# Performance work log

Hardware: AMD Instinct MI355X
Metric: run time of the kernel (lower is better)

## Reference

```python
import jax, jax.numpy as jnp
import numpy as np

D_MODEL = 1024
N_HEADS = 16
HEAD_DIM = D_MODEL // N_HEADS


def setup_inputs() -> dict:
    key = jax.random.key(0)
    ks = jax.random.split(key, 5)
    B, S = 2, 2048
    x = jax.random.normal(ks[0], (B, S, D_MODEL), dtype=jnp.float32)
    # nn.Linear weights: [out_features, in_features]
    s_in = 1.0 / np.sqrt(D_MODEL)
    qkv_w = jax.random.uniform(ks[1], (3 * D_MODEL, D_MODEL), jnp.float32, -s_in, s_in)
    qkv_b = jax.random.uniform(ks[2], (3 * D_MODEL,), jnp.float32, -s_in, s_in)
    out_w = jax.random.uniform(ks[3], (D_MODEL, D_MODEL), jnp.float32, -s_in, s_in)
    out_b = jax.random.uniform(ks[4], (D_MODEL,), jnp.float32, -s_in, s_in)
    return {"x": x, "qkv_w": qkv_w, "qkv_b": qkv_b, "out_w": out_w, "out_b": out_b}


def reference(x, qkv_w, qkv_b, out_w, out_b):
    B, S, D = x.shape
    H, Hd = N_HEADS, HEAD_DIM
    scale = 1.0 / np.sqrt(Hd)
    qkv = jnp.einsum('bsd,ed->bse', x, qkv_w) + qkv_b  # [B,S,3D]
    qkv = qkv.reshape(B, S, 3, H, Hd)
    q = qkv[:, :, 0].transpose(0, 2, 1, 3)  # [B,H,S,Hd]
    k = qkv[:, :, 1].transpose(0, 2, 1, 3)
    v = qkv[:, :, 2].transpose(0, 2, 1, 3)
    scores = jnp.einsum('bhqd,bhkd->bhqk', q, k) * scale  # [B,H,S,S]
    causal = jnp.triu(jnp.ones((S, S), dtype=bool), k=1)
    scores = jnp.where(causal[None, None], -jnp.inf, scores)
    probs = jax.nn.softmax(scores, axis=-1)
    out = jnp.einsum('bhqk,bhkd->bhqd', probs, v)  # [B,H,S,Hd]
    out = out.transpose(0, 2, 1, 3).reshape(B, S, D)
    out = jnp.einsum('bsd,ed->bse', out, out_w) + out_b
    return out
```

## Files before the change

kernel.cpp:

```cpp
#include <hip/hip_runtime.h>
#include <hip/hip_bf16.h>

#define SEQ    2048
#define DMODEL 1024
#define NHEAD  16
#define HDIM   64
#define BATCH  2
#define NTOK   (BATCH * SEQ)

#define N_X   (NTOK * DMODEL)
#define N_WQ  (3 * DMODEL * DMODEL)
#define N_BQ  (3 * DMODEL)
#define N_WO  (DMODEL * DMODEL)
#define N_BO  (DMODEL)
#define N_CANON (N_X + N_WQ + N_BQ + N_WO + N_BO)

#define NEG_SENT (-1.0e30f)
#define QSCALE 0.1803368801111f

typedef __attribute__((ext_vector_type(8))) short short8;
typedef __attribute__((ext_vector_type(4))) short short4v;
typedef __attribute__((ext_vector_type(4))) float f32x4;

#define MFMA_BF16(A, B, C) __builtin_amdgcn_mfma_f32_16x16x32_bf16((A), (B), (C), 0, 0, 0)

static __device__ __forceinline__ short8 load8(const __hip_bfloat16* p) {
    return *(const short8*)p;
}

static __device__ __forceinline__ void async16(const void* g, void* l) {
    __builtin_amdgcn_global_load_lds(
        (const __attribute__((address_space(1))) unsigned int*)g,
        (__attribute__((address_space(3))) unsigned int*)l,
        16, 0, 0);
}

__global__ void detect_kernel(const unsigned short* __restrict__ w, int* flag) {
    int cnt = 0;
    for (int i = threadIdx.x; i < 512; i += 64) {
        const unsigned e = (w[i] >> 7) & 0xFF;
        if (e >= 125) cnt++;
    }
#pragma unroll
    for (int o = 32; o; o >>= 1) cnt += __shfl_down(cnt, o);
    if (threadIdx.x == 0) *flag = (cnt > 8) ? 1 : 0;
}

__global__ __launch_bounds__(256) void canon_kernel(
    const void* __restrict__ s0, const void* __restrict__ s1,
    const void* __restrict__ s2, const void* __restrict__ s3,
    const void* __restrict__ s4,
    __hip_bfloat16* __restrict__ dst, const int* __restrict__ flag)
{
    const int idx = blockIdx.x * 256 + threadIdx.x;
    if (idx >= N_CANON) return;
    const void* src;
    int off;
    if (idx < N_X)                         { src = s0; off = idx; }
    else if (idx < N_X + N_WQ)             { src = s1; off = idx - N_X; }
    else if (idx < N_X + N_WQ + N_BQ)      { src = s2; off = idx - (N_X + N_WQ); }
    else if (idx < N_X + N_WQ + N_BQ + N_WO){ src = s3; off = idx - (N_X + N_WQ + N_BQ); }
    else                                   { src = s4; off = idx - (N_X + N_WQ + N_BQ + N_WO); }
    const bool isf32 = (*flag != 0);
    const float v = isf32 ? ((const float*)src)[off]
                          : __bfloat162float(((const __hip_bfloat16*)src)[off]);
    dst[idx] = __float2bfloat16(v);
}

__global__ __launch_bounds__(256) void qkv_gemm_kernel(
    const __hip_bfloat16* __restrict__ X,
    const __hip_bfloat16* __restrict__ W,
    const __hip_bfloat16* __restrict__ bias,
    __hip_bfloat16* __restrict__ Qs,
    __hip_bfloat16* __restrict__ Kb,
    __hip_bfloat16* __restrict__ Vt)
{
    constexpr int Kd = DMODEL;
    __shared__ __align__(16) __hip_bfloat16 As[2][128 * 32];
    __shared__ __align__(16) __hip_bfloat16 Bs[2][128 * 32];

    const int tid   = threadIdx.x;
    const int lane  = tid & 63;
    const int w     = tid >> 6;
    const int mTile = blockIdx.y * 128;
    const int nTile = blockIdx.x * 128;
    const int wm    = (w >> 1) * 64;
    const int wn    = (w & 1) * 64;
    const int lm    = lane & 15;
    const int lk    = (lane >> 4) * 8;

    f32x4 acc[4][4];
#pragma unroll
    for (int i = 0; i < 4; ++i)
#pragma unroll
        for (int j = 0; j < 4; ++j)
            acc[i][j] = (f32x4){0.f, 0.f, 0.f, 0.f};

    const int r0c = tid >> 2, p0c = tid & 3;
    const int r1c = (tid + 256) >> 2;

    const __hip_bfloat16* gA0 = &X[(size_t)(mTile + r0c) * Kd + p0c * 8];
    const __hip_bfloat16* gA1 = &X[(size_t)(mTile + r1c) * Kd + p0c * 8];
    const __hip_bfloat16* gB0 = &W[(size_t)(nTile + r0c) * Kd + p0c * 8];
    const __hip_bfloat16* gB1 = &W[(size_t)(nTile + r1c) * Kd + p0c * 8];

    async16(gA0, (char*)As[0] + tid * 16);
    async16(gA1, (char*)As[0] + tid * 16 + 4096);
    async16(gB0, (char*)Bs[0] + tid * 16);
    async16(gB1, (char*)Bs[0] + tid * 16 + 4096);

    int cur = 0;
    constexpr int NIT = Kd / 32;
    for (int it = 0; it < NIT; ++it) {
        if (it + 1 < NIT) {
            const int k1 = (it + 1) * 32;
            async16(gA0 + k1, (char*)As[cur ^ 1] + tid * 16);
            async16(gA1 + k1, (char*)As[cur ^ 1] + tid * 16 + 4096);
            async16(gB0 + k1, (char*)Bs[cur ^ 1] + tid * 16);
            async16(gB1 + k1, (char*)Bs[cur ^ 1] + tid * 16 + 4096);
            asm volatile("s_waitcnt vmcnt(4)" ::: "memory");
        } else {
            asm volatile("s_waitcnt vmcnt(0)" ::: "memory");
        }
        __builtin_amdgcn_s_barrier();
        __builtin_amdgcn_sched_barrier(0);

        const __hip_bfloat16* Ac = As[cur];
        const __hip_bfloat16* Bc = Bs[cur];
        short8 a[4], b[4];
#pragma unroll
        for (int i = 0; i < 4; ++i)
            a[i] = *(const short8*)&Ac[(wm + i * 16 + lm) * 32 + lk];
#pragma unroll
        for (int j = 0; j < 4; ++j)
            b[j] = *(const short8*)&Bc[(wn + j * 16 + lm) * 32 + lk];
#pragma unroll
        for (int i = 0; i < 4; ++i)
#pragma unroll
            for (int j = 0; j < 4; ++j)
                acc[i][j] = MFMA_BF16(a[i], b[j], acc[i][j]);

        __builtin_amdgcn_s_barrier();
        cur ^= 1;
    }

    const int r0 = (lane >> 4) * 4;
#pragma unroll
    for (int j = 0; j < 4; ++j) {
        const int n  = nTile + wn + j * 16 + lm;
        const float bv = __bfloat162float(bias[n]);
        const int c = n >> 10;
        const int h = (n >> 6) & 15;
        const int d = n & 63;
#pragma unroll
        for (int i = 0; i < 4; ++i) {
            if (c == 2) {
                const int m0 = mTile + wm + i * 16 + r0;
                const int bb = m0 >> 11;
                const int s0 = m0 & (SEQ - 1);
                const int bh = bb * NHEAD + h;
                short4v pk;
#pragma unroll
                for (int r = 0; r < 4; ++r)
                    pk[r] = (short)__bfloat16_as_ushort(
                        __float2bfloat16(acc[i][j][r] + bv));
                *(short4v*)&Vt[(size_t)(bh * HDIM + d) * SEQ + s0] = pk;
            } else {
#pragma unroll
                for (int r = 0; r < 4; ++r) {
                    const int m  = mTile + wm + i * 16 + r0 + r;
                    const int bb = m >> 11;
                    const int s  = m & (SEQ - 1);
                    const int bh = bb * NHEAD + h;
                    const float v = acc[i][j][r] + bv;
                    if (c == 0) {
                        Qs[(size_t)(bh * SEQ + s) * HDIM + d] = __float2bfloat16(v * QSCALE);
                    } else {
                        Kb[(size_t)(bh * SEQ + s) * HDIM + d] = __float2bfloat16(v);
                    }
                }
            }
        }
    }
}

#define P_PITCH 72
__global__ __launch_bounds__(512, 4) void attn_kernel(
    const __hip_bfloat16* __restrict__ Qs,
    const __hip_bfloat16* __restrict__ Kb,
    const __hip_bfloat16* __restrict__ Vt,
    float* __restrict__ Opart,
    float* __restrict__ MLpart)
{
    __shared__ __align__(16) __hip_bfloat16 Kt[3][64 * 64];
    __shared__ __align__(16) __hip_bfloat16 Vs[3][64 * 64];
    __shared__ __align__(16) __hip_bfloat16 Pall[8][16 * P_PITCH];

    const int tid  = threadIdx.x;
    const int lane = tid & 63;
    const int wv   = tid >> 6;
    const int p    = blockIdx.x >> 1;
    const int kh   = blockIdx.x & 1;
    const int bh   = blockIdx.y;
    const int wgid = bh * 16 + blockIdx.x;

    const int lm  = lane & 15;
    const int q4  = lane >> 4;
    const int lk  = q4 * 8;
    const int swz = (lm & 3) << 4;

    __hip_bfloat16* P = Pall[wv];

    const __hip_bfloat16* Qbh = Qs + (size_t)bh * SEQ * HDIM;
    const __hip_bfloat16* Kbh = Kb + (size_t)bh * SEQ * HDIM;
    const __hip_bfloat16* Vbh = Vt + (size_t)bh * HDIM * SEQ;

    const int srow = tid >> 3;
    const int scb  = (tid & 7) ^ (srow & 7);

    for (int ph = 0; ph < 2; ++ph) {
        const int qb    = ph ? p : 15 - p;
        const int wbase = qb * 128 + wv * 16;
        const int nCh   = qb + 1;
        const int c0    = kh * nCh;

        short8 qa[2];
#pragma unroll
        for (int h = 0; h < 2; ++h)
            qa[h] = load8(&Qbh[(size_t)(wbase + lm) * HDIM + h * 32 + lk]);

        float m_run = NEG_SENT;
        float l_run = 0.f;
        f32x4 Oacc[4];
#pragma unroll
        for (int t = 0; t < 4; ++t) Oacc[t] = (f32x4){0.f, 0.f, 0.f, 0.f};

        __builtin_amdgcn_s_barrier();

        {
            const int kk0 = c0 * 64;
            async16(&Kbh[(size_t)(kk0 + srow) * HDIM + scb * 8], (char*)Kt[0] + tid * 16);
            async16(&Vbh[(size_t)srow * SEQ + kk0 + scb * 8],    (char*)Vs[0] + tid * 16);
            if (nCh >= 2) {
                const int kk1 = kk0 + 64;
                async16(&Kbh[(size_t)(kk1 + srow) * HDIM + scb * 8], (char*)Kt[1] + tid * 16);
                async16(&Vbh[(size_t)srow * SEQ + kk1 + scb * 8],    (char*)Vs[1] + tid * 16);
            }
        }

        int cur = 0;
        for (int ci = 0; ci < nCh; ++ci) {
            const int k0 = (c0 + ci) * 64;

            if (ci + 1 < nCh) {
                asm volatile("s_waitcnt vmcnt(2)" ::: "memory");
            } else {
                asm volatile("s_waitcnt vmcnt(0)" ::: "memory");
            }
            __builtin_amdgcn_s_barrier();
            __builtin_amdgcn_sched_barrier(0);

            if (ci + 2 < nCh) {
                const int slot = (cur + 2 >= 3) ? cur - 1 : cur + 2;
                const int kk = (c0 + ci + 2) * 64;
                async16(&Kbh[(size_t)(kk + srow) * HDIM + scb * 8], (char*)Kt[slot] + tid * 16);
                async16(&Vbh[(size_t)srow * SEQ + kk + scb * 8],    (char*)Vs[slot] + tid * 16);
            }

            if (k0 <= wbase + 15) {
                const __hip_bfloat16* Kc = Kt[cur];
                const __hip_bfloat16* Vc = Vs[cur];

                short8 ka[4][2];
#pragma unroll
                for (int t = 0; t < 4; ++t)
#pragma unroll
                    for (int h = 0; h < 2; ++h)
                        ka[t][h] = *(const short8*)&Kc[(t * 16 + lm) * 64 +
                                                       (((h * 4 + q4) ^ (lm & 7)) * 8)];

                f32x4 sc[4];
#pragma unroll
                for (int t = 0; t < 4; ++t) sc[t] = (f32x4){0.f, 0.f, 0.f, 0.f};
#pragma unroll
                for (int t = 0; t < 4; ++t) {
                    sc[t] = MFMA_BF16(ka[t][0], qa[0], sc[t]);
                    sc[t] = MFMA_BF16(ka[t][1], qa[1], sc[t]);
                }

                if (k0 + 63 > wbase) {
                    const int row = wbase + lm;
#pragma unroll
                    for (int t = 0; t < 4; ++t)
#pragma unroll
                        for (int r = 0; r < 4; ++r) {
                            const int key = k0 + t * 16 + q4 * 4 + r;
                            if (key > row) sc[t][r] = NEG_SENT;
                        }
                }

                float mx = sc[0][0];
#pragma unroll
                for (int t = 0; t < 4; ++t)
#pragma unroll
                    for (int r = 0; r < 4; ++r) mx = fmaxf(mx, sc[t][r]);
                mx = fmaxf(mx, __shfl_xor(mx, 16));
                mx = fmaxf(mx, __shfl_xor(mx, 32));

                if (!__all(mx <= m_run + 8.0f)) {
                    const float mn = fmaxf(m_run, mx);
                    const float alpha = exp2f(m_run - mn);
                    m_run = mn;
                    l_run *= alpha;
#pragma unroll
                    for (int r = 0; r < 4; ++r) {
                        const float av = __shfl(alpha, q4 * 4 + r);
#pragma unroll
                        for (int t = 0; t < 4; ++t) Oacc[t][r] *= av;
                    }
                }

                float s = 0.f;
#pragma unroll
                for (int t = 0; t < 4; ++t)
#pragma unroll
                    for (int r = 0; r < 4; ++r) {
                        const float pv = exp2f(sc[t][r] - m_run);
                        sc[t][r] = pv;
                        s += pv;
                    }
                s += __shfl_xor(s, 16);
                s += __shfl_xor(s, 32);
                l_run += s;

#pragma unroll
                for (int t = 0; t < 4; ++t) {
                    short4v pk;
#pragma unroll
                    for (int r = 0; r < 4; ++r)
                        pk[r] = (short)__bfloat16_as_ushort(__float2bfloat16(sc[t][r]));
                    const int col = (t * 16 + q4 * 4) ^ swz;
                    *(short4v*)&P[lm * P_PITCH + col] = pk;
                }

#pragma unroll
                for (int h = 0; h < 2; ++h) {
                    const short8 pa = *(const short8*)&P[lm * P_PITCH + ((h * 32 + lk) ^ swz)];
#pragma unroll
                    for (int t = 0; t < 4; ++t) {
                        const short8 vb = *(const short8*)&Vc[(t * 16 + lm) * 64 +
                                                              (((h * 4 + q4) ^ (lm & 7)) * 8)];
                        Oacc[t] = MFMA_BF16(pa, vb, Oacc[t]);
                    }
                }
            }

            cur = (cur + 1 == 3) ? 0 : cur + 1;
        }

        const size_t pbase = ((size_t)wgid * 2 + ph) * 128;
#pragma unroll
        for (int t = 0; t < 4; ++t)
#pragma unroll
            for (int r = 0; r < 4; ++r)
                Opart[(pbase + wv * 16 + q4 * 4 + r) * 64 + t * 16 + lm] = Oacc[t][r];
        if (lane < 16) {
            MLpart[(pbase + wv * 16 + lane) * 2 + 0] = m_run;
            MLpart[(pbase + wv * 16 + lane) * 2 + 1] = l_run;
        }
    }
}

__global__ __launch_bounds__(256) void attn_merge_kernel(
    const float* __restrict__ Opart, const float* __restrict__ MLpart,
    __hip_bfloat16* __restrict__ O)
{
    const int idx  = blockIdx.x * 256 + threadIdx.x;
    const int d16  = idx & 3;
    const int grow = idx >> 2;
    const int bh   = grow >> 11;
    const int s    = grow & 2047;
    const int qb   = s >> 7;
    const int rin  = s & 127;
    const int p    = (qb >= 8) ? (15 - qb) : qb;
    const int ph   = (qb >= 8) ? 0 : 1;
    const size_t r0 = ((size_t)(bh * 16 + p * 2 + 0) * 2 + ph) * 128 + rin;
    const size_t r1 = ((size_t)(bh * 16 + p * 2 + 1) * 2 + ph) * 128 + rin;

    const float m1 = MLpart[r0 * 2], l1 = MLpart[r0 * 2 + 1];
    const float m2 = MLpart[r1 * 2], l2 = MLpart[r1 * 2 + 1];
    const float mm = fmaxf(m1, m2);
    const float a1 = exp2f(m1 - mm), a2 = exp2f(m2 - mm);
    const float inv = 1.0f / (a1 * l1 + a2 * l2);

    const f32x4* O1 = (const f32x4*)&Opart[r0 * 64 + d16 * 16];
    const f32x4* O2 = (const f32x4*)&Opart[r1 * 64 + d16 * 16];

    short8 out[2];
#pragma unroll
    for (int v = 0; v < 4; ++v) {
        const f32x4 x1 = O1[v], x2 = O2[v];
#pragma unroll
        for (int j = 0; j < 4; ++j)
            out[v >> 1][(v & 1) * 4 + j] = (short)__bfloat16_as_ushort(
                __float2bfloat16((a1 * x1[j] + a2 * x2[j]) * inv));
    }
    const int b = bh >> 4, hh = bh & 15;
    __hip_bfloat16* dst = &O[((size_t)b * SEQ + s) * DMODEL + hh * 64 + d16 * 16];
    ((short8*)dst)[0] = out[0];
    ((short8*)dst)[1] = out[1];
}

__global__ __launch_bounds__(256) void proj_gemm_kernel(
    const __hip_bfloat16* __restrict__ A,
    const __hip_bfloat16* __restrict__ W,
    const __hip_bfloat16* __restrict__ bias,
    void* __restrict__ outv,
    const int* __restrict__ flag)
{
    constexpr int Kd = DMODEL;
    __shared__ __align__(16) __hip_bfloat16 As[2][128 * 32];
    __shared__ __align__(16) __hip_bfloat16 Bs[2][64 * 32];

    const int tid   = threadIdx.x;
    const int lane  = tid & 63;
    const int w     = tid >> 6;
    const int mTile = blockIdx.y * 128;
    const int nTile = blockIdx.x * 64;
    const int wm    = (w >> 1) * 64;
    const int wn    = (w & 1) * 32;
    const int lm    = lane & 15;
    const int lk    = (lane >> 4) * 8;
    const bool f32out = (*flag != 0);

    f32x4 acc[4][2];
#pragma unroll
    for (int i = 0; i < 4; ++i)
#pragma unroll
        for (int j = 0; j < 2; ++j)
            acc[i][j] = (f32x4){0.f, 0.f, 0.f, 0.f};

    const int r0c = tid >> 2, p0c = tid & 3;
    const int r1c = (tid + 256) >> 2;

    const __hip_bfloat16* gA0 = &A[(size_t)(mTile + r0c) * Kd + p0c * 8];
    const __hip_bfloat16* gA1 = &A[(size_t)(mTile + r1c) * Kd + p0c * 8];
    const __hip_bfloat16* gB0 = &W[(size_t)(nTile + r0c) * Kd + p0c * 8];

    async16(gA0, (char*)As[0] + tid * 16);
    async16(gA1, (char*)As[0] + tid * 16 + 4096);
    async16(gB0, (char*)Bs[0] + tid * 16);

    int cur = 0;
    constexpr int NIT = Kd / 32;
    for (int it = 0; it < NIT; ++it) {
        if (it + 1 < NIT) {
            const int k1 = (it + 1) * 32;
            async16(gA0 + k1, (char*)As[cur ^ 1] + tid * 16);
            async16(gA1 + k1, (char*)As[cur ^ 1] + tid * 16 + 4096);
            async16(gB0 + k1, (char*)Bs[cur ^ 1] + tid * 16);
            asm volatile("s_waitcnt vmcnt(3)" ::: "memory");
        } else {
            asm volatile("s_waitcnt vmcnt(0)" ::: "memory");
        }
        __builtin_amdgcn_s_barrier();
        __builtin_amdgcn_sched_barrier(0);

        const __hip_bfloat16* Ac = As[cur];
        const __hip_bfloat16* Bc = Bs[cur];
        short8 a[4], b[2];
#pragma unroll
        for (int i = 0; i < 4; ++i)
            a[i] = *(const short8*)&Ac[(wm + i * 16 + lm) * 32 + lk];
#pragma unroll
        for (int j = 0; j < 2; ++j)
            b[j] = *(const short8*)&Bc[(wn + j * 16 + lm) * 32 + lk];
#pragma unroll
        for (int i = 0; i < 4; ++i)
#pragma unroll
            for (int j = 0; j < 2; ++j)
                acc[i][j] = MFMA_BF16(a[i], b[j], acc[i][j]);

        __builtin_amdgcn_s_barrier();
        cur ^= 1;
    }

    const int r0 = (lane >> 4) * 4;
#pragma unroll
    for (int j = 0; j < 2; ++j) {
        const int n = nTile + wn + j * 16 + lm;
        const float bv = __bfloat162float(bias[n]);
#pragma unroll
        for (int i = 0; i < 4; ++i) {
#pragma unroll
            for (int r = 0; r < 4; ++r) {
                const size_t m = mTile + wm + i * 16 + r0 + r;
                const float v = acc[i][j][r] + bv;
                if (f32out) ((float*)outv)[m * DMODEL + n] = v;
                else ((__hip_bfloat16*)outv)[m * DMODEL + n] = __float2bfloat16(v);
            }
        }
    }
}

extern "C" void kernel_launch(void* const* d_in, const int* in_sizes, int n_in,
                              void* d_out, int out_size, void* d_ws, size_t ws_size,
                              hipStream_t stream) {
    const size_t OFF_CANON = 256;
    const size_t OFF_QS = OFF_CANON + (size_t)N_CANON * 2;
    const size_t OFF_KB = OFF_QS + (size_t)NTOK * DMODEL * 2;
    const size_t OFF_VT = OFF_KB + (size_t)NTOK * DMODEL * 2;
    const size_t OFF_AO = OFF_VT + (size_t)NTOK * DMODEL * 2;
    const size_t OFF_OP = OFF_AO + (size_t)NTOK * DMODEL * 2;
    const size_t OFF_ML = OFF_OP + (size_t)512 * 2 * 128 * 64 * 4;

    char* wsb = (char*)d_ws;
    int* flag = (int*)wsb;
    __hip_bfloat16* canon = (__hip_bfloat16*)(wsb + OFF_CANON);
    __hip_bfloat16* Xc = canon;
    __hip_bfloat16* Wq = Xc + N_X;
    __hip_bfloat16* Bq = Wq + N_WQ;
    __hip_bfloat16* Wo = Bq + N_BQ;
    __hip_bfloat16* Bo = Wo + N_WO;
    __hip_bfloat16* Qs = (__hip_bfloat16*)(wsb + OFF_QS);
    __hip_bfloat16* Kb = (__hip_bfloat16*)(wsb + OFF_KB);
    __hip_bfloat16* Vt = (__hip_bfloat16*)(wsb + OFF_VT);
    __hip_bfloat16* Ao = (__hip_bfloat16*)(wsb + OFF_AO);
    float* Opart = (float*)(wsb + OFF_OP);
    float* MLpart = (float*)(wsb + OFF_ML);

    detect_kernel<<<1, 64, 0, stream>>>((const unsigned short*)d_in[1], flag);
    canon_kernel<<<(N_CANON + 255) / 256, 256, 0, stream>>>(
        d_in[0], d_in[1], d_in[2], d_in[3], d_in[4], canon, flag);

    {
        dim3 grid(3 * DMODEL / 128, NTOK / 128);
        qkv_gemm_kernel<<<grid, 256, 0, stream>>>(Xc, Wq, Bq, Qs, Kb, Vt);
    }
    {
        dim3 grid(16, BATCH * NHEAD);
        attn_kernel<<<grid, 512, 0, stream>>>(Qs, Kb, Vt, Opart, MLpart);
        attn_merge_kernel<<<(NTOK * NHEAD * 4) / 256, 256, 0, stream>>>(
            Opart, MLpart, Ao);
    }
    {
        dim3 grid(DMODEL / 64, NTOK / 128);
        proj_gemm_kernel<<<grid, 256, 0, stream>>>(Ao, Wo, Bo, d_out, flag);
    }
}
```

Before: 198.6 us.

## Vectorize input conversion, swizzle GEMM LDS tiles, and raise MFMA priority in attention

```diff
diff --git a/kernel.cpp b/kernel.cpp
--- a/kernel.cpp
+++ b/kernel.cpp
@@ -52,19 +52,29 @@
     const void* __restrict__ s4,
     __hip_bfloat16* __restrict__ dst, const int* __restrict__ flag)
 {
-    const int idx = blockIdx.x * 256 + threadIdx.x;
-    if (idx >= N_CANON) return;
+    const int v = blockIdx.x * 256 + threadIdx.x;
+    if (v >= N_CANON / 8) return;
+    const int idx = v * 8;
     const void* src;
     int off;
-    if (idx < N_X)                         { src = s0; off = idx; }
-    else if (idx < N_X + N_WQ)             { src = s1; off = idx - N_X; }
-    else if (idx < N_X + N_WQ + N_BQ)      { src = s2; off = idx - (N_X + N_WQ); }
+    if (idx < N_X)                          { src = s0; off = idx; }
+    else if (idx < N_X + N_WQ)              { src = s1; off = idx - N_X; }
+    else if (idx < N_X + N_WQ + N_BQ)       { src = s2; off = idx - (N_X + N_WQ); }
     else if (idx < N_X + N_WQ + N_BQ + N_WO){ src = s3; off = idx - (N_X + N_WQ + N_BQ); }
-    else                                   { src = s4; off = idx - (N_X + N_WQ + N_BQ + N_WO); }
-    const bool isf32 = (*flag != 0);
-    const float v = isf32 ? ((const float*)src)[off]
-                          : __bfloat162float(((const __hip_bfloat16*)src)[off]);
-    dst[idx] = __float2bfloat16(v);
+    else                                    { src = s4; off = idx - (N_X + N_WQ + N_BQ + N_WO); }
+    if (*flag != 0) {
+        const f32x4* sp = (const f32x4*)((const float*)src + off);
+        const f32x4 x0 = sp[0], x1 = sp[1];
+        short8 o;
+#pragma unroll
+        for (int j = 0; j < 4; ++j) {
+            o[j]     = (short)__bfloat16_as_ushort(__float2bfloat16(x0[j]));
+            o[4 + j] = (short)__bfloat16_as_ushort(__float2bfloat16(x1[j]));
+        }
+        *(short8*)&dst[idx] = o;
+    } else {
+        *(short8*)&dst[idx] = *(const short8*)((const __hip_bfloat16*)src + off);
+    }
 }
 
 __global__ __launch_bounds__(256) void qkv_gemm_kernel(
@@ -87,7 +97,8 @@
     const int wm    = (w >> 1) * 64;
     const int wn    = (w & 1) * 64;
     const int lm    = lane & 15;
-    const int lk    = (lane >> 4) * 8;
+    const int q4    = lane >> 4;
+    const int lks   = (q4 ^ ((lm >> 1) & 3)) * 8;
 
     f32x4 acc[4][4];
 #pragma unroll
@@ -96,13 +107,14 @@
         for (int j = 0; j < 4; ++j)
             acc[i][j] = (f32x4){0.f, 0.f, 0.f, 0.f};
 
-    const int r0c = tid >> 2, p0c = tid & 3;
+    const int r0c = tid >> 2;
     const int r1c = (tid + 256) >> 2;
-
-    const __hip_bfloat16* gA0 = &X[(size_t)(mTile + r0c) * Kd + p0c * 8];
-    const __hip_bfloat16* gA1 = &X[(size_t)(mTile + r1c) * Kd + p0c * 8];
-    const __hip_bfloat16* gB0 = &W[(size_t)(nTile + r0c) * Kd + p0c * 8];
-    const __hip_bfloat16* gB1 = &W[(size_t)(nTile + r1c) * Kd + p0c * 8];
+    const int cbs = ((tid & 3) ^ ((tid >> 3) & 3)) * 8;
+
+    const __hip_bfloat16* gA0 = &X[(size_t)(mTile + r0c) * Kd + cbs];
+    const __hip_bfloat16* gA1 = &X[(size_t)(mTile + r1c) * Kd + cbs];
+    const __hip_bfloat16* gB0 = &W[(size_t)(nTile + r0c) * Kd + cbs];
+    const __hip_bfloat16* gB1 = &W[(size_t)(nTile + r1c) * Kd + cbs];
 
     async16(gA0, (char*)As[0] + tid * 16);
     async16(gA1, (char*)As[0] + tid * 16 + 4096);
@@ -130,10 +142,10 @@
         short8 a[4], b[4];
 #pragma unroll
         for (int i = 0; i < 4; ++i)
-            a[i] = *(const short8*)&Ac[(wm + i * 16 + lm) * 32 + lk];
+            a[i] = *(const short8*)&Ac[(wm + i * 16 + lm) * 32 + lks];
 #pragma unroll
         for (int j = 0; j < 4; ++j)
-            b[j] = *(const short8*)&Bc[(wn + j * 16 + lm) * 32 + lk];
+            b[j] = *(const short8*)&Bc[(wn + j * 16 + lm) * 32 + lks];
 #pragma unroll
         for (int i = 0; i < 4; ++i)
 #pragma unroll
@@ -282,11 +294,13 @@
                 f32x4 sc[4];
 #pragma unroll
                 for (int t = 0; t < 4; ++t) sc[t] = (f32x4){0.f, 0.f, 0.f, 0.f};
+                __builtin_amdgcn_s_setprio(1);
 #pragma unroll
                 for (int t = 0; t < 4; ++t) {
                     sc[t] = MFMA_BF16(ka[t][0], qa[0], sc[t]);
                     sc[t] = MFMA_BF16(ka[t][1], qa[1], sc[t]);
                 }
+                __builtin_amdgcn_s_setprio(0);
 
                 if (k0 + 63 > wbase) {
                     const int row = wbase + lm;
@@ -343,6 +357,7 @@
                     *(short4v*)&P[lm * P_PITCH + col] = pk;
                 }
 
+                __builtin_amdgcn_s_setprio(1);
 #pragma unroll
                 for (int h = 0; h < 2; ++h) {
                     const short8 pa = *(const short8*)&P[lm * P_PITCH + ((h * 32 + lk) ^ swz)];
@@ -353,6 +368,7 @@
                         Oacc[t] = MFMA_BF16(pa, vb, Oacc[t]);
                     }
                 }
+                __builtin_amdgcn_s_setprio(0);
             }
 
             cur = (cur + 1 == 3) ? 0 : cur + 1;
@@ -430,7 +446,8 @@
     const int wm    = (w >> 1) * 64;
     const int wn    = (w & 1) * 32;
     const int lm    = lane & 15;
-    const int lk    = (lane >> 4) * 8;
+    const int q4    = lane >> 4;
+    const int lks   = (q4 ^ ((lm >> 1) & 3)) * 8;
     const bool f32out = (*flag != 0);
 
     f32x4 acc[4][2];
@@ -440,12 +457,13 @@
         for (int j = 0; j < 2; ++j)
             acc[i][j] = (f32x4){0.f, 0.f, 0.f, 0.f};
 
-    const int r0c = tid >> 2, p0c = tid & 3;
+    const int r0c = tid >> 2;
     const int r1c = (tid + 256) >> 2;
-
-    const __hip_bfloat16* gA0 = &A[(size_t)(mTile + r0c) * Kd + p0c * 8];
-    const __hip_bfloat16* gA1 = &A[(size_t)(mTile + r1c) * Kd + p0c * 8];
-    const __hip_bfloat16* gB0 = &W[(size_t)(nTile + r0c) * Kd + p0c * 8];
+    const int cbs = ((tid & 3) ^ ((tid >> 3) & 3)) * 8;
+
+    const __hip_bfloat16* gA0 = &A[(size_t)(mTile + r0c) * Kd + cbs];
+    const __hip_bfloat16* gA1 = &A[(size_t)(mTile + r1c) * Kd + cbs];
+    const __hip_bfloat16* gB0 = &W[(size_t)(nTile + r0c) * Kd + cbs];
 
     async16(gA0, (char*)As[0] + tid * 16);
     async16(gA1, (char*)As[0] + tid * 16 + 4096);
@@ -471,10 +489,10 @@
         short8 a[4], b[2];
 #pragma unroll
         for (int i = 0; i < 4; ++i)
-            a[i] = *(const short8*)&Ac[(wm + i * 16 + lm) * 32 + lk];
+            a[i] = *(const short8*)&Ac[(wm + i * 16 + lm) * 32 + lks];
 #pragma unroll
         for (int j = 0; j < 2; ++j)
-            b[j] = *(const short8*)&Bc[(wn + j * 16 + lm) * 32 + lk];
+            b[j] = *(const short8*)&Bc[(wn + j * 16 + lm) * 32 + lks];
 #pragma unroll
         for (int i = 0; i < 4; ++i)
 #pragma unroll
@@ -530,7 +548,7 @@
     float* MLpart = (float*)(wsb + OFF_ML);
 
     detect_kernel<<<1, 64, 0, stream>>>((const unsigned short*)d_in[1], flag);
-    canon_kernel<<<(N_CANON + 255) / 256, 256, 0, stream>>>(
+    canon_kernel<<<(N_CANON / 8 + 255) / 256, 256, 0, stream>>>(
         d_in[0], d_in[1], d_in[2], d_in[3], d_in[4], canon, flag);
 
     {
```

After: 192.2 us. 3.2% less time.
